# Optimization experiments

Hardware: AMD Instinct MI355X
Metric: run time of the kernel (lower is better)

Reference implementation:

```python
import jax, jax.numpy as jnp
import numpy as np

D_MODEL, NHEAD, INT_DIM = 1024, 16, 4096
HEAD_DIM = D_MODEL // NHEAD
EPS = 1e-5


def _layernorm(x, gamma, beta):
    mu = jnp.mean(x, axis=-1, keepdims=True)
    var = jnp.var(x, axis=-1, keepdims=True)
    return (x - mu) * jax.lax.rsqrt(var + EPS) * gamma + beta


def setup_inputs() -> dict:
    key = jax.random.key(0)
    ks = jax.random.split(key, 16)
    B, T = 2, 2048
    s = 0.02
    inp = {
        'x': jax.random.normal(ks[0], (B, T, D_MODEL), dtype=jnp.float32),
        'Wq': jax.random.normal(ks[1], (D_MODEL, D_MODEL), dtype=jnp.float32) * s,
        'bq': jnp.zeros((D_MODEL,), jnp.float32),
        'Wk': jax.random.normal(ks[2], (D_MODEL, D_MODEL), dtype=jnp.float32) * s,
        'bk': jnp.zeros((D_MODEL,), jnp.float32),
        'Wv': jax.random.normal(ks[3], (D_MODEL, D_MODEL), dtype=jnp.float32) * s,
        'bv': jnp.zeros((D_MODEL,), jnp.float32),
        'Wo': jax.random.normal(ks[4], (D_MODEL, D_MODEL), dtype=jnp.float32) * s,
        'bo': jnp.zeros((D_MODEL,), jnp.float32),
        'ln1_g': jnp.ones((D_MODEL,), jnp.float32),
        'ln1_b': jnp.zeros((D_MODEL,), jnp.float32),
        'ln2_g': jnp.ones((D_MODEL,), jnp.float32),
        'ln2_b': jnp.zeros((D_MODEL,), jnp.float32),
        'W1': jax.random.normal(ks[5], (D_MODEL, INT_DIM), dtype=jnp.float32) * s,
        'b1': jnp.zeros((INT_DIM,), jnp.float32),
        'W2': jax.random.normal(ks[6], (INT_DIM, D_MODEL), dtype=jnp.float32) * s,
        'b2': jnp.zeros((D_MODEL,), jnp.float32),
    }
    return inp


def reference(x, Wq, bq, Wk, bk, Wv, bv, Wo, bo, ln1_g, ln1_b, ln2_g, ln2_b, W1, b1, W2, b2):
    B, T, D = x.shape
    # projections
    q = (x @ Wq + bq).reshape(B, T, NHEAD, HEAD_DIM).transpose(0, 2, 1, 3)
    k = (x @ Wk + bk).reshape(B, T, NHEAD, HEAD_DIM).transpose(0, 2, 1, 3)
    v = (x @ Wv + bv).reshape(B, T, NHEAD, HEAD_DIM).transpose(0, 2, 1, 3)
    # attention: [B,H,T,T] scores, softmax over keys
    scores = jnp.einsum('bhqd,bhkd->bhqk', q, k) / jnp.sqrt(jnp.float32(HEAD_DIM))
    attn = jax.nn.softmax(scores, axis=-1)
    out = jnp.einsum('bhqk,bhkd->bhqd', attn, v)
    out = out.transpose(0, 2, 1, 3).reshape(B, T, D)
    attn_output = out @ Wo + bo
    # residual + layernorm 1
    h = _layernorm(x + attn_output, ln1_g, ln1_b)
    # FFN
    ff = jax.nn.relu(h @ W1 + b1) @ W2 + b2
    # residual + layernorm 2
    return _layernorm(h + ff, ln2_g, ln2_b)
```

## Files before the change

### kernel.cpp

```cpp
#include <hip/hip_runtime.h>
#include <cstdint>

#define DEVI __device__ __forceinline__

typedef float f32x4 __attribute__((ext_vector_type(4)));
typedef __bf16 bf16x8 __attribute__((ext_vector_type(8)));
typedef unsigned int u32x4v __attribute__((ext_vector_type(4)));
typedef unsigned short u16;
typedef unsigned int u32;
typedef unsigned long long u64;

#define LOG2E 1.44269504088896f
#define QSCALE (0.125f * LOG2E)

DEVI u16 bf16bits(float f) {
    u32 u = __builtin_bit_cast(u32, f);
    u32 r = u + 0x7fffu + ((u >> 16) & 1u);
    return (u16)(r >> 16);
}

DEVI float bf2f(u16 v) {
    u32 u = (u32)v << 16;
    return __builtin_bit_cast(float, u);
}

DEVI u32 pack2bf(float a, float b) {
    u16 x = __builtin_bit_cast(u16, (__bf16)a);
    u16 y = __builtin_bit_cast(u16, (__bf16)b);
    return (u32)x | ((u32)y << 16);
}

DEVI float ex2(float x) {
    float r;
    asm("v_exp_f32 %0, %1" : "=v"(r) : "v"(x));
    return r;
}

DEVI void gload16(const void* g, const void* l) {
    __builtin_amdgcn_global_load_lds(
        (const __attribute__((address_space(1))) void*)(u64)(uintptr_t)g,
        (__attribute__((address_space(3))) void*)(u32)(uintptr_t)l,
        16, 0, 0);
}

__global__ __launch_bounds__(256)
void prep_kernel(const float* __restrict__ x, u16* __restrict__ xb,
                 const float* __restrict__ Wq, const float* __restrict__ Wk,
                 const float* __restrict__ Wv, const float* __restrict__ Wo,
                 u16* __restrict__ Wqt, u16* __restrict__ Wkt,
                 u16* __restrict__ Wvt, u16* __restrict__ Wot,
                 const float* __restrict__ W1, u16* __restrict__ W1t,
                 const float* __restrict__ W2, u16* __restrict__ W2t) {
    __shared__ float t[64][65];
    const int b = blockIdx.x;
    const int tid = threadIdx.x;
    if (b < 4096) {
        int i = b * 256 + tid;
        float4 v = ((const float4*)x)[i];
        ((uint2*)xb)[i] = make_uint2(pack2bf(v.x, v.y), pack2bf(v.z, v.w));
        return;
    }
    const float* src;
    u16* dst;
    int K_, N_, k0, n0;
    if (b < 5120) {
        int l = b - 4096;
        int z = l >> 8;
        l &= 255;
        src = z == 0 ? Wq : z == 1 ? Wk : z == 2 ? Wv : Wo;
        dst = z == 0 ? Wqt : z == 1 ? Wkt : z == 2 ? Wvt : Wot;
        K_ = 1024; N_ = 1024;
        k0 = (l & 15) * 64; n0 = (l >> 4) * 64;
    } else if (b < 6144) {
        int l = b - 5120;
        src = W1; dst = W1t; K_ = 1024; N_ = 4096;
        k0 = (l & 15) * 64; n0 = (l >> 4) * 64;
    } else {
        int l = b - 6144;
        src = W2; dst = W2t; K_ = 4096; N_ = 1024;
        k0 = (l & 63) * 64; n0 = (l >> 6) * 64;
    }
#pragma unroll
    for (int i = 0; i < 16; i++) {
        int idx = i * 256 + tid;
        int r = idx >> 6, c = idx & 63;
        t[r][c] = src[(u64)(k0 + r) * N_ + n0 + c];
    }
    __syncthreads();
#pragma unroll
    for (int i = 0; i < 16; i++) {
        int idx = i * 256 + tid;
        int r = idx >> 6, c = idx & 63;
        dst[(u64)(n0 + r) * K_ + k0 + c] = bf16bits(t[c][r]);
    }
}

enum { MODE_QK = 0, MODE_VT = 1, MODE_RESID = 2, MODE_RELU = 3 };

DEVI void gemm_core(const u16* __restrict__ A, const u16* __restrict__ Bt, int K_,
                    u16 (*ldsA)[128 * 64], u16 (*ldsB)[128 * 64],
                    f32x4 (&acc)[4][4], int m0, int n0) {
    const int tid = threadIdx.x;
    const int lane = tid & 63;
    const int wid = tid >> 6;
    const int wr = wid >> 1, wc = wid & 1;
    const int l15 = lane & 15, l4 = lane >> 4;
    const int srow = tid >> 3;
    const int sc = (tid & 7) ^ (srow & 7);

    const u16* ap[4];
    const u16* bp[4];
#pragma unroll
    for (int i = 0; i < 4; i++) {
        ap[i] = A + (u64)(m0 + i * 32 + srow) * K_ + sc * 8;
        bp[i] = Bt + (u64)(n0 + i * 32 + srow) * K_ + sc * 8;
    }

    auto stageA = [&](int buf) {
#pragma unroll
        for (int i = 0; i < 4; i++) {
            gload16(ap[i], (const char*)ldsA[buf] + (i * 256 + tid) * 16);
            ap[i] += 64;
        }
    };
    auto stageB = [&](int buf) {
#pragma unroll
        for (int i = 0; i < 4; i++) {
            gload16(bp[i], (const char*)ldsB[buf] + (i * 256 + tid) * 16);
            bp[i] += 64;
        }
    };

    auto compute = [&](const u16* A_, const u16* B_) {
#pragma unroll
        for (int ks = 0; ks < 2; ks++) {
            bf16x8 af[4], bfr[4];
#pragma unroll
            for (int mi = 0; mi < 4; mi++) {
                int row = wr * 64 + mi * 16 + l15;
                af[mi] = *(const bf16x8*)((const char*)A_ + row * 128 +
                                          (((ks * 4 + l4) ^ (row & 7)) * 16));
            }
#pragma unroll
            for (int ni = 0; ni < 4; ni++) {
                int row = wc * 64 + ni * 16 + l15;
                bfr[ni] = *(const bf16x8*)((const char*)B_ + row * 128 +
                                           (((ks * 4 + l4) ^ (row & 7)) * 16));
            }
            __builtin_amdgcn_s_setprio(1);
#pragma unroll
            for (int mi = 0; mi < 4; mi++)
#pragma unroll
                for (int ni = 0; ni < 4; ni++)
                    acc[mi][ni] = __builtin_amdgcn_mfma_f32_16x16x32_bf16(
                        af[mi], bfr[ni], acc[mi][ni], 0, 0, 0);
            __builtin_amdgcn_s_setprio(0);
        }
    };

    const int nk = K_ >> 6;
    stageA(0);
    stageB(0);
    stageA(1);
    int ca = 0, cbb = 0, sa = 2, sb = 1;
    for (int t = 0; t < nk; t++) {
        if (t < nk - 1) {
            asm volatile("s_waitcnt vmcnt(4)" ::: "memory");
        } else {
            asm volatile("s_waitcnt vmcnt(0)" ::: "memory");
        }
        __builtin_amdgcn_s_barrier();
        if (t + 1 < nk) { stageB(sb); sb ^= 1; }
        if (t + 2 < nk) { stageA(sa); sa = (sa == 2) ? 0 : sa + 1; }
        compute(ldsA[ca], ldsB[cbb]);
        ca = (ca == 2) ? 0 : ca + 1;
        cbb ^= 1;
    }
}

template <int MODE>
DEVI void gemm_epilogue(f32x4 (&acc)[4][4], const float* __restrict__ bias,
                        const float* __restrict__ resid, void* __restrict__ outp,
                        int N_, int m0, int n0, float scale) {
    const int tid = threadIdx.x;
    const int lane = tid & 63;
    const int wid = tid >> 6;
    const int wr = wid >> 1, wc = wid & 1;
    const int l15 = lane & 15, l4 = lane >> 4;
#pragma unroll
    for (int mi = 0; mi < 4; mi++) {
#pragma unroll
        for (int ni = 0; ni < 4; ni++) {
            const int n = n0 + wc * 64 + ni * 16 + l15;
            const float bv = bias[n];
            const int mb = m0 + wr * 64 + mi * 16 + l4 * 4;
            if (MODE == MODE_VT) {
                const int b = mb >> 11, t = mb & 2047;
                const int hh = n >> 6, d = n & 63;
                u32 lo = pack2bf(acc[mi][ni][0] + bv, acc[mi][ni][1] + bv);
                u32 hi = pack2bf(acc[mi][ni][2] + bv, acc[mi][ni][3] + bv);
                u64 idx = ((u64)((b << 4) + hh) * 64 + d) * 2048 + t;
                *(uint2*)((u16*)outp + idx) = make_uint2(lo, hi);
            } else {
#pragma unroll
                for (int r = 0; r < 4; r++) {
                    const int m = mb + r;
                    const float v = acc[mi][ni][r] + bv;
                    if (MODE == MODE_QK) {
                        const int b = m >> 11, t = m & 2047;
                        const int hh = n >> 6, d = n & 63;
                        ((u16*)outp)[(((u64)((b << 4) + hh) * 2048 + t) << 6) + d] =
                            bf16bits(v * scale);
                    } else if (MODE == MODE_RESID) {
                        const u64 i2 = (u64)m * N_ + n;
                        ((float*)outp)[i2] = v + resid[i2];
                    } else {
                        ((u16*)outp)[(u64)m * N_ + n] = bf16bits(fmaxf(v, 0.f));
                    }
                }
            }
        }
    }
}

template <int MODE>
__global__ __launch_bounds__(256, 2)
void gemm_kernel(const u16* __restrict__ A, const u16* __restrict__ Bt,
                 const float* __restrict__ bias, const float* __restrict__ resid,
                 void* __restrict__ outp, int N_, int K_) {
    __shared__ u16 ldsA[3][128 * 64];
    __shared__ u16 ldsB[2][128 * 64];
    const int m0 = blockIdx.x * 128;
    const int n0 = blockIdx.y * 128;
    f32x4 acc[4][4];
#pragma unroll
    for (int i = 0; i < 4; i++)
#pragma unroll
        for (int j = 0; j < 4; j++) acc[i][j] = (f32x4){0.f, 0.f, 0.f, 0.f};
    gemm_core(A, Bt, K_, ldsA, ldsB, acc, m0, n0);
    gemm_epilogue<MODE>(acc, bias, resid, outp, N_, m0, n0, 1.f);
}

__global__ __launch_bounds__(256, 2)
void gemm_qkv_kernel(const u16* __restrict__ A,
                     const u16* __restrict__ Wq, const u16* __restrict__ Wk,
                     const u16* __restrict__ Wv,
                     const float* __restrict__ bq, const float* __restrict__ bk,
                     const float* __restrict__ bv,
                     u16* __restrict__ Qo, u16* __restrict__ Ko, u16* __restrict__ Vo) {
    __shared__ u16 ldsA[3][128 * 64];
    __shared__ u16 ldsB[2][128 * 64];
    const int z = blockIdx.z;
    const u16* Bt = z == 0 ? Wq : z == 1 ? Wk : Wv;
    const float* bias = z == 0 ? bq : z == 1 ? bk : bv;
    const int m0 = blockIdx.x * 128;
    const int n0 = blockIdx.y * 128;
    f32x4 acc[4][4];
#pragma unroll
    for (int i = 0; i < 4; i++)
#pragma unroll
        for (int j = 0; j < 4; j++) acc[i][j] = (f32x4){0.f, 0.f, 0.f, 0.f};
    gemm_core(A, Bt, 1024, ldsA, ldsB, acc, m0, n0);
    if (z == 2)
        gemm_epilogue<MODE_VT>(acc, bias, nullptr, Vo, 1024, m0, n0, 1.f);
    else
        gemm_epilogue<MODE_QK>(acc, bias, nullptr, z == 0 ? Qo : Ko, 1024, m0, n0,
                               z == 0 ? QSCALE : 1.f);
}

template <bool RB16>
__global__ __launch_bounds__(256, 2)
void gemm64_kernel(const u16* __restrict__ A, const u16* __restrict__ Bt,
                   const float* __restrict__ bias, const void* __restrict__ resid,
                   float* __restrict__ outp, int K_) {
    __shared__ u16 ldsA[3][128 * 64];
    __shared__ u16 ldsB[3][64 * 64];
    const int tid = threadIdx.x;
    const int lane = tid & 63;
    const int wid = tid >> 6;
    const int m0 = blockIdx.x * 128;
    const int n0 = blockIdx.y * 64;
    const int l15 = lane & 15, l4 = lane >> 4;
    const int srow = tid >> 3;
    const int sc = (tid & 7) ^ (srow & 7);

    const u16* ap[4];
    const u16* bp[2];
#pragma unroll
    for (int i = 0; i < 4; i++)
        ap[i] = A + (u64)(m0 + i * 32 + srow) * K_ + sc * 8;
#pragma unroll
    for (int i = 0; i < 2; i++)
        bp[i] = Bt + (u64)(n0 + i * 32 + srow) * K_ + sc * 8;

    auto stage = [&](int buf) {
#pragma unroll
        for (int i = 0; i < 4; i++) {
            gload16(ap[i], (const char*)ldsA[buf] + (i * 256 + tid) * 16);
            ap[i] += 64;
        }
#pragma unroll
        for (int i = 0; i < 2; i++) {
            gload16(bp[i], (const char*)ldsB[buf] + (i * 256 + tid) * 16);
            bp[i] += 64;
        }
    };

    f32x4 acc[2][4];
#pragma unroll
    for (int i = 0; i < 2; i++)
#pragma unroll
        for (int j = 0; j < 4; j++) acc[i][j] = (f32x4){0.f, 0.f, 0.f, 0.f};

    auto compute = [&](const u16* A_, const u16* B_) {
#pragma unroll
        for (int ks = 0; ks < 2; ks++) {
            bf16x8 af[2], bfr[4];
#pragma unroll
            for (int mi = 0; mi < 2; mi++) {
                int row = wid * 32 + mi * 16 + l15;
                af[mi] = *(const bf16x8*)((const char*)A_ + row * 128 +
                                          (((ks * 4 + l4) ^ (row & 7)) * 16));
            }
#pragma unroll
            for (int ni = 0; ni < 4; ni++) {
                int row = ni * 16 + l15;
                bfr[ni] = *(const bf16x8*)((const char*)B_ + row * 128 +
                                           (((ks * 4 + l4) ^ (row & 7)) * 16));
            }
            __builtin_amdgcn_s_setprio(1);
#pragma unroll
            for (int mi = 0; mi < 2; mi++)
#pragma unroll
                for (int ni = 0; ni < 4; ni++)
                    acc[mi][ni] = __builtin_amdgcn_mfma_f32_16x16x32_bf16(
                        af[mi], bfr[ni], acc[mi][ni], 0, 0, 0);
            __builtin_amdgcn_s_setprio(0);
        }
    };

    const int nk = K_ >> 6;
    stage(0);
    stage(1);
    int cb = 0, sb = 2;
    for (int t = 0; t < nk; t++) {
        if (t < nk - 1) {
            asm volatile("s_waitcnt vmcnt(6)" ::: "memory");
        } else {
            asm volatile("s_waitcnt vmcnt(0)" ::: "memory");
        }
        __builtin_amdgcn_s_barrier();
        if (t + 2 < nk) stage(sb);
        compute(ldsA[cb], ldsB[cb]);
        cb = (cb == 2) ? 0 : cb + 1;
        sb = (sb == 2) ? 0 : sb + 1;
    }

#pragma unroll
    for (int mi = 0; mi < 2; mi++) {
#pragma unroll
        for (int ni = 0; ni < 4; ni++) {
            const int n = n0 + ni * 16 + l15;
            const float bv = bias[n];
            const int mb = m0 + wid * 32 + mi * 16 + l4 * 4;
#pragma unroll
            for (int r = 0; r < 4; r++) {
                const u64 i2 = (u64)(mb + r) * 1024 + n;
                const float rv = RB16 ? bf2f(((const u16*)resid)[i2])
                                      : ((const float*)resid)[i2];
                outp[i2] = acc[mi][ni][r] + bv + rv;
            }
        }
    }
}

__global__ __launch_bounds__(256, 3)
void attn_kernel(const u16* __restrict__ Qg, const u16* __restrict__ Kg,
                 const u16* __restrict__ Vtg, u16* __restrict__ Og) {
    __shared__ u16 ldsK[3][64 * 64];
    __shared__ u16 ldsV[3][64 * 64];
    const int tid = threadIdx.x;
    const int lane = tid & 63;
    const int w = tid >> 6;
    const int l15 = lane & 15, l4 = lane >> 4;
    const int id = blockIdx.x;
    const int swz = (id & 7) * 128 + (id >> 3);
    const int bh = swz >> 5;
    const int qblk = swz & 31;
    const u64 kvbase = (u64)bh * 2048 * 64;
    const int qw0 = qblk * 64 + w * 16;

    const int srow = tid >> 3;
    const int sc8 = ((tid & 7) ^ (srow & 7)) * 8;
    const u16* kq0 = Kg + kvbase + (u64)srow * 64 + sc8;
    const u16* kq1 = Kg + kvbase + (u64)(srow + 32) * 64 + sc8;
    const u16* vq0 = Vtg + kvbase + (u64)srow * 2048 + sc8;
    const u16* vq1 = Vtg + kvbase + (u64)(srow + 32) * 2048 + sc8;

    auto stage = [&](int buf) {
        gload16(kq0, (const char*)ldsK[buf] + tid * 16);
        gload16(kq1, (const char*)ldsK[buf] + (256 + tid) * 16);
        gload16(vq0, (const char*)ldsV[buf] + tid * 16);
        gload16(vq1, (const char*)ldsV[buf] + (256 + tid) * 16);
        kq0 += 4096; kq1 += 4096; vq0 += 64; vq1 += 64;
    };

    bf16x8 aq[2];
#pragma unroll
    for (int ks = 0; ks < 2; ks++)
        aq[ks] = *(const bf16x8*)(Qg + kvbase + (u64)(qw0 + l15) * 64 + ks * 32 + l4 * 8);
    asm volatile("s_waitcnt vmcnt(0)" ::: "memory");

    stage(0);
    stage(1);

    const u32x4v onesw = {0x3F803F80u, 0x3F803F80u, 0x3F803F80u, 0x3F803F80u};
    const bf16x8 aones = __builtin_bit_cast(bf16x8, onesw);

    f32x4 acco[4];
#pragma unroll
    for (int i = 0; i < 4; i++) acco[i] = (f32x4){0.f, 0.f, 0.f, 0.f};
    f32x4 lacc = (f32x4){0.f, 0.f, 0.f, 0.f};

    auto tile_body = [&](const u16* K_, const u16* V_) {
        f32x4 sf[4];
#pragma unroll
        for (int f = 0; f < 4; f++) sf[f] = (f32x4){0.f, 0.f, 0.f, 0.f};
#pragma unroll
        for (int ks = 0; ks < 2; ks++) {
            bf16x8 ak[4];
#pragma unroll
            for (int f = 0; f < 4; f++) {
                int row = f * 16 + l15;
                ak[f] = *(const bf16x8*)((const char*)K_ + row * 128 +
                                         (((ks * 4 + l4) ^ (row & 7)) * 16));
            }
            __builtin_amdgcn_s_setprio(1);
#pragma unroll
            for (int f = 0; f < 4; f++)
                sf[f] = __builtin_amdgcn_mfma_f32_16x16x32_bf16(ak[f], aq[ks], sf[f], 0, 0, 0);
            __builtin_amdgcn_s_setprio(0);
        }

        u32 A[4], B[4];
#pragma unroll
        for (int f = 0; f < 4; f++) {
            float p0 = ex2(sf[f][0]);
            float p1 = ex2(sf[f][1]);
            float p2 = ex2(sf[f][2]);
            float p3 = ex2(sf[f][3]);
            A[f] = pack2bf(p0, p1);
            B[f] = pack2bf(p2, p3);
        }
        asm volatile("v_permlane32_swap_b32 %0, %1" : "+v"(A[0]), "+v"(A[1]));
        asm volatile("v_permlane16_swap_b32 %0, %1" : "+v"(A[0]), "+v"(A[1]));
        asm volatile("v_permlane32_swap_b32 %0, %1" : "+v"(B[0]), "+v"(B[1]));
        asm volatile("v_permlane16_swap_b32 %0, %1" : "+v"(B[0]), "+v"(B[1]));
        asm volatile("v_permlane32_swap_b32 %0, %1" : "+v"(A[2]), "+v"(A[3]));
        asm volatile("v_permlane16_swap_b32 %0, %1" : "+v"(A[2]), "+v"(A[3]));
        asm volatile("v_permlane32_swap_b32 %0, %1" : "+v"(B[2]), "+v"(B[3]));
        asm volatile("v_permlane16_swap_b32 %0, %1" : "+v"(B[2]), "+v"(B[3]));

#pragma unroll
        for (int ks = 0; ks < 2; ks++) {
            u32x4v pw = {A[2 * ks], B[2 * ks], A[2 * ks + 1], B[2 * ks + 1]};
            bf16x8 pfrag = __builtin_bit_cast(bf16x8, pw);
            bf16x8 av[4];
#pragma unroll
            for (int nf = 0; nf < 4; nf++) {
                int row = nf * 16 + l15;
                av[nf] = *(const bf16x8*)((const char*)V_ + row * 128 +
                                          (((ks * 4 + l4) ^ (row & 7)) * 16));
            }
            __builtin_amdgcn_s_setprio(1);
            lacc = __builtin_amdgcn_mfma_f32_16x16x32_bf16(aones, pfrag, lacc, 0, 0, 0);
#pragma unroll
            for (int nf = 0; nf < 4; nf++)
                acco[nf] = __builtin_amdgcn_mfma_f32_16x16x32_bf16(av[nf], pfrag, acco[nf], 0, 0, 0);
            __builtin_amdgcn_s_setprio(0);
        }
    };

    int cb = 0;
    int sb = 2;
    for (int t = 0; t < 31; t++) {
        asm volatile("s_waitcnt vmcnt(4)" ::: "memory");
        __builtin_amdgcn_s_barrier();
        if (t < 30) stage(sb);
        tile_body(ldsK[cb], ldsV[cb]);
        cb = (cb == 2) ? 0 : cb + 1;
        sb = (sb == 2) ? 0 : sb + 1;
    }
    asm volatile("s_waitcnt vmcnt(0)" ::: "memory");
    __builtin_amdgcn_s_barrier();
    tile_body(ldsK[cb], ldsV[cb]);

    const float inv = 1.f / lacc[0];

    const int b = bh >> 4, h = bh & 15;
    const int tq = qw0 + l15;
#pragma unroll
    for (int nf = 0; nf < 4; nf++) {
        const int d = nf * 16 + l4 * 4;
        u32 lo = pack2bf(acco[nf][0] * inv, acco[nf][1] * inv);
        u32 hi = pack2bf(acco[nf][2] * inv, acco[nf][3] * inv);
        *(uint2*)(Og + ((u64)(b * 2048 + tq) << 10) + h * 64 + d) = make_uint2(lo, hi);
    }
}

template <bool WF32, bool WB16>
__global__ __launch_bounds__(256, 4)
void ln_kernel(const float* __restrict__ in, const float* __restrict__ gam,
               const float* __restrict__ bet, float* __restrict__ outf,
               u16* __restrict__ outb) {
    __shared__ float red[2][4];
    const int row = blockIdx.x;
    const int tid = threadIdx.x;
    float4 v = ((const float4*)(in + (u64)row * 1024))[tid];
    float s = v.x + v.y + v.z + v.w;
    float sq = v.x * v.x + v.y * v.y + v.z * v.z + v.w * v.w;
#pragma unroll
    for (int sh = 1; sh < 64; sh <<= 1) {
        s += __shfl_xor(s, sh, 64);
        sq += __shfl_xor(sq, sh, 64);
    }
    if ((tid & 63) == 0) { red[0][tid >> 6] = s; red[1][tid >> 6] = sq; }
    __syncthreads();
    s = red[0][0] + red[0][1] + red[0][2] + red[0][3];
    sq = red[1][0] + red[1][1] + red[1][2] + red[1][3];
    float mu = s * (1.f / 1024.f);
    float var = sq * (1.f / 1024.f) - mu * mu;
    float inv = rsqrtf(var + 1e-5f);
    float4 g = ((const float4*)gam)[tid];
    float4 bb = ((const float4*)bet)[tid];
    float4 o;
    o.x = (v.x - mu) * inv * g.x + bb.x;
    o.y = (v.y - mu) * inv * g.y + bb.y;
    o.z = (v.z - mu) * inv * g.z + bb.z;
    o.w = (v.w - mu) * inv * g.w + bb.w;
    if (WF32) ((float4*)(outf + (u64)row * 1024))[tid] = o;
    if (WB16) {
        ((uint2*)(outb + (u64)row * 1024))[tid] = make_uint2(pack2bf(o.x, o.y), pack2bf(o.z, o.w));
    }
}

extern "C" void kernel_launch(void* const* d_in, const int* in_sizes, int n_in,
                              void* d_out, int out_size, void* d_ws, size_t ws_size,
                              hipStream_t stream) {
    (void)in_sizes; (void)n_in; (void)out_size; (void)ws_size;
    const float* x  = (const float*)d_in[0];
    const float* Wq = (const float*)d_in[1];
    const float* bq = (const float*)d_in[2];
    const float* Wk = (const float*)d_in[3];
    const float* bk = (const float*)d_in[4];
    const float* Wv = (const float*)d_in[5];
    const float* bv = (const float*)d_in[6];
    const float* Wo = (const float*)d_in[7];
    const float* bo = (const float*)d_in[8];
    const float* g1 = (const float*)d_in[9];
    const float* be1 = (const float*)d_in[10];
    const float* g2 = (const float*)d_in[11];
    const float* be2 = (const float*)d_in[12];
    const float* W1 = (const float*)d_in[13];
    const float* b1 = (const float*)d_in[14];
    const float* W2 = (const float*)d_in[15];
    const float* b2 = (const float*)d_in[16];

    char* ws = (char*)d_ws;
    const u64 MB = 1024ull * 1024ull;
    u16* xb    = (u16*)(ws + 0);
    u16* Wqt   = (u16*)(ws + 8 * MB);
    u16* Wkt   = (u16*)(ws + 10 * MB);
    u16* Wvt   = (u16*)(ws + 12 * MB);
    u16* Wot   = (u16*)(ws + 14 * MB);
    u16* W1t   = (u16*)(ws + 16 * MB);
    u16* W2t   = (u16*)(ws + 24 * MB);
    u16* Qb    = (u16*)(ws + 32 * MB);
    u16* Kb    = (u16*)(ws + 40 * MB);
    u16* Vtb   = (u16*)(ws + 48 * MB);
    u16* Ob    = (u16*)(ws + 56 * MB);
    float* pre1 = (float*)(ws + 64 * MB);
    u16* hb    = (u16*)(ws + 96 * MB);
    u16* ffb   = (u16*)(ws + 104 * MB);
    float* pre2 = (float*)(ws + 80 * MB);

    prep_kernel<<<7168, 256, 0, stream>>>(x, xb, Wq, Wk, Wv, Wo,
                                          Wqt, Wkt, Wvt, Wot, W1, W1t, W2, W2t);

    gemm_qkv_kernel<<<dim3(32, 8, 3), 256, 0, stream>>>(xb, Wqt, Wkt, Wvt,
                                                        bq, bk, bv, Qb, Kb, Vtb);

    attn_kernel<<<1024, 256, 0, stream>>>(Qb, Kb, Vtb, Ob);

    gemm64_kernel<false><<<dim3(32, 16), 256, 0, stream>>>(Ob, Wot, bo, x, pre1, 1024);
    ln_kernel<false, true><<<4096, 256, 0, stream>>>(pre1, g1, be1, nullptr, hb);
    gemm_kernel<MODE_RELU><<<dim3(32, 32), 256, 0, stream>>>(hb, W1t, b1, nullptr, ffb, 4096, 1024);
    gemm64_kernel<true><<<dim3(32, 16), 256, 0, stream>>>(ffb, W2t, b2, hb, pre2, 4096);
    ln_kernel<true, false><<<4096, 256, 0, stream>>>(pre2, g2, be2, (float*)d_out, nullptr);
}
```

Baseline: 202.2 us.

## Stage GEMM epilogues through LDS for coalesced vectorized global stores

GEMM epilogues now write the accumulators into shared memory, reusing the operand LDS buffers, and then read them back in row-contiguous chunks so each thread issues 16-byte global stores. This covers the Q/K/Vt head layouts, the ReLU output and the fp32 residual outputs, and the residual and bias loads become vectorized too. The weight-transpose prep kernel also packs four bf16 values per store instead of writing scalars. The cost is extra barriers and an LDS round trip per tile, with padded strides added to limit bank conflicts.

```diff
diff --git a/kernel.cpp b/kernel.cpp
--- a/kernel.cpp
+++ b/kernel.cpp
@@ -88,14 +88,17 @@
     }
     __syncthreads();
 #pragma unroll
-    for (int i = 0; i < 16; i++) {
+    for (int i = 0; i < 4; i++) {
         int idx = i * 256 + tid;
-        int r = idx >> 6, c = idx & 63;
-        dst[(u64)(n0 + r) * K_ + k0 + c] = bf16bits(t[c][r]);
-    }
-}
-
-enum { MODE_QK = 0, MODE_VT = 1, MODE_RESID = 2, MODE_RELU = 3 };
+        int cq = idx & 15;
+        int r = idx >> 4;
+        u32 lo = (u32)bf16bits(t[cq * 4 + 0][r]) | ((u32)bf16bits(t[cq * 4 + 1][r]) << 16);
+        u32 hi = (u32)bf16bits(t[cq * 4 + 2][r]) | ((u32)bf16bits(t[cq * 4 + 3][r]) << 16);
+        *(uint2*)(dst + (u64)(n0 + r) * K_ + k0 + cq * 4) = make_uint2(lo, hi);
+    }
+}
+
+enum { MODE_QK = 0, MODE_VT = 1, MODE_RELU = 3 };
 
 DEVI void gemm_core(const u16* __restrict__ A, const u16* __restrict__ Bt, int K_,
                     u16 (*ldsA)[128 * 64], u16 (*ldsB)[128 * 64],
@@ -180,45 +183,55 @@
 
 template <int MODE>
 DEVI void gemm_epilogue(f32x4 (&acc)[4][4], const float* __restrict__ bias,
-                        const float* __restrict__ resid, void* __restrict__ outp,
-                        int N_, int m0, int n0, float scale) {
+                        void* __restrict__ outp, int N_, int m0, int n0,
+                        float scale, u16* l16) {
     const int tid = threadIdx.x;
     const int lane = tid & 63;
     const int wid = tid >> 6;
     const int wr = wid >> 1, wc = wid & 1;
     const int l15 = lane & 15, l4 = lane >> 4;
+    __syncthreads();
 #pragma unroll
     for (int mi = 0; mi < 4; mi++) {
 #pragma unroll
         for (int ni = 0; ni < 4; ni++) {
-            const int n = n0 + wc * 64 + ni * 16 + l15;
-            const float bv = bias[n];
-            const int mb = m0 + wr * 64 + mi * 16 + l4 * 4;
+            const int nl = wc * 64 + ni * 16 + l15;
+            const int mlb = wr * 64 + mi * 16 + l4 * 4;
+            const float bv = bias[n0 + nl];
             if (MODE == MODE_VT) {
-                const int b = mb >> 11, t = mb & 2047;
-                const int hh = n >> 6, d = n & 63;
                 u32 lo = pack2bf(acc[mi][ni][0] + bv, acc[mi][ni][1] + bv);
                 u32 hi = pack2bf(acc[mi][ni][2] + bv, acc[mi][ni][3] + bv);
-                u64 idx = ((u64)((b << 4) + hh) * 64 + d) * 2048 + t;
-                *(uint2*)((u16*)outp + idx) = make_uint2(lo, hi);
+                *(uint2*)(l16 + nl * 136 + mlb) = make_uint2(lo, hi);
             } else {
 #pragma unroll
                 for (int r = 0; r < 4; r++) {
-                    const int m = mb + r;
-                    const float v = acc[mi][ni][r] + bv;
-                    if (MODE == MODE_QK) {
-                        const int b = m >> 11, t = m & 2047;
-                        const int hh = n >> 6, d = n & 63;
-                        ((u16*)outp)[(((u64)((b << 4) + hh) * 2048 + t) << 6) + d] =
-                            bf16bits(v * scale);
-                    } else if (MODE == MODE_RESID) {
-                        const u64 i2 = (u64)m * N_ + n;
-                        ((float*)outp)[i2] = v + resid[i2];
-                    } else {
-                        ((u16*)outp)[(u64)m * N_ + n] = bf16bits(fmaxf(v, 0.f));
-                    }
+                    float v = acc[mi][ni][r] + bv;
+                    if (MODE == MODE_RELU) v = fmaxf(v, 0.f);
+                    else v = v * scale;
+                    l16[(mlb + r) * 136 + nl] = bf16bits(v);
                 }
             }
+        }
+    }
+    __syncthreads();
+#pragma unroll
+    for (int it = 0; it < 8; it++) {
+        int c = it * 256 + tid;
+        int rr = c >> 4, nc = c & 15;
+        u32x4v v = *(const u32x4v*)(l16 + rr * 136 + nc * 8);
+        if (MODE == MODE_QK) {
+            int m = m0 + rr;
+            int b = m >> 11, t = m & 2047;
+            int hh = (n0 >> 6) + (nc >> 3);
+            int d = (nc & 7) * 8;
+            *(u32x4v*)((u16*)outp + (((u64)((b << 4) + hh) * 2048 + t) << 6) + d) = v;
+        } else if (MODE == MODE_VT) {
+            int hh = (n0 + rr) >> 6;
+            int d = (n0 + rr) & 63;
+            int b = m0 >> 11, tb = m0 & 2047;
+            *(u32x4v*)((u16*)outp + ((u64)((b << 4) + hh) * 64 + d) * 2048 + tb + nc * 8) = v;
+        } else {
+            *(u32x4v*)((u16*)outp + (u64)(m0 + rr) * N_ + n0 + nc * 8) = v;
         }
     }
 }
@@ -226,8 +239,8 @@
 template <int MODE>
 __global__ __launch_bounds__(256, 2)
 void gemm_kernel(const u16* __restrict__ A, const u16* __restrict__ Bt,
-                 const float* __restrict__ bias, const float* __restrict__ resid,
-                 void* __restrict__ outp, int N_, int K_) {
+                 const float* __restrict__ bias, void* __restrict__ outp,
+                 int N_, int K_) {
     __shared__ u16 ldsA[3][128 * 64];
     __shared__ u16 ldsB[2][128 * 64];
     const int m0 = blockIdx.x * 128;
@@ -238,7 +251,7 @@
 #pragma unroll
         for (int j = 0; j < 4; j++) acc[i][j] = (f32x4){0.f, 0.f, 0.f, 0.f};
     gemm_core(A, Bt, K_, ldsA, ldsB, acc, m0, n0);
-    gemm_epilogue<MODE>(acc, bias, resid, outp, N_, m0, n0, 1.f);
+    gemm_epilogue<MODE>(acc, bias, outp, N_, m0, n0, 1.f, (u16*)ldsA);
 }
 
 __global__ __launch_bounds__(256, 2)
@@ -262,10 +275,10 @@
         for (int j = 0; j < 4; j++) acc[i][j] = (f32x4){0.f, 0.f, 0.f, 0.f};
     gemm_core(A, Bt, 1024, ldsA, ldsB, acc, m0, n0);
     if (z == 2)
-        gemm_epilogue<MODE_VT>(acc, bias, nullptr, Vo, 1024, m0, n0, 1.f);
+        gemm_epilogue<MODE_VT>(acc, bias, Vo, 1024, m0, n0, 1.f, (u16*)ldsA);
     else
-        gemm_epilogue<MODE_QK>(acc, bias, nullptr, z == 0 ? Qo : Ko, 1024, m0, n0,
-                               z == 0 ? QSCALE : 1.f);
+        gemm_epilogue<MODE_QK>(acc, bias, z == 0 ? Qo : Ko, 1024, m0, n0,
+                               z == 0 ? QSCALE : 1.f, (u16*)ldsA);
 }
 
 template <bool RB16>
@@ -356,21 +369,42 @@
         sb = (sb == 2) ? 0 : sb + 1;
     }
 
+    float* fl = (float*)ldsA;
+    __syncthreads();
 #pragma unroll
     for (int mi = 0; mi < 2; mi++) {
 #pragma unroll
         for (int ni = 0; ni < 4; ni++) {
-            const int n = n0 + ni * 16 + l15;
-            const float bv = bias[n];
-            const int mb = m0 + wid * 32 + mi * 16 + l4 * 4;
-#pragma unroll
-            for (int r = 0; r < 4; r++) {
-                const u64 i2 = (u64)(mb + r) * 1024 + n;
-                const float rv = RB16 ? bf2f(((const u16*)resid)[i2])
-                                      : ((const float*)resid)[i2];
-                outp[i2] = acc[mi][ni][r] + bv + rv;
-            }
-        }
+            const int nl = ni * 16 + l15;
+            const int mlb = wid * 32 + mi * 16 + l4 * 4;
+#pragma unroll
+            for (int r = 0; r < 4; r++)
+                fl[(mlb + r) * 68 + nl] = acc[mi][ni][r];
+        }
+    }
+    __syncthreads();
+#pragma unroll
+    for (int it = 0; it < 8; it++) {
+        int c = it * 256 + tid;
+        int rr = c >> 4, nc = c & 15;
+        f32x4 v = *(const f32x4*)(fl + rr * 68 + nc * 4);
+        const int n = n0 + nc * 4;
+        float4 bv = *(const float4*)(bias + n);
+        const u64 i2 = (u64)(m0 + rr) * 1024 + n;
+        float4 rv;
+        if (RB16) {
+            uint2 rb = *(const uint2*)((const u16*)resid + i2);
+            rv.x = bf2f((u16)(rb.x & 0xffffu)); rv.y = bf2f((u16)(rb.x >> 16));
+            rv.z = bf2f((u16)(rb.y & 0xffffu)); rv.w = bf2f((u16)(rb.y >> 16));
+        } else {
+            rv = *(const float4*)((const float*)resid + i2);
+        }
+        float4 o;
+        o.x = v[0] + bv.x + rv.x;
+        o.y = v[1] + bv.y + rv.y;
+        o.z = v[2] + bv.z + rv.z;
+        o.w = v[3] + bv.w + rv.w;
+        *(float4*)(outp + i2) = o;
     }
 }
 
@@ -594,7 +628,7 @@
 
     gemm64_kernel<false><<<dim3(32, 16), 256, 0, stream>>>(Ob, Wot, bo, x, pre1, 1024);
     ln_kernel<false, true><<<4096, 256, 0, stream>>>(pre1, g1, be1, nullptr, hb);
-    gemm_kernel<MODE_RELU><<<dim3(32, 32), 256, 0, stream>>>(hb, W1t, b1, nullptr, ffb, 4096, 1024);
+    gemm_kernel<MODE_RELU><<<dim3(32, 32), 256, 0, stream>>>(hb, W1t, b1, ffb, 4096, 1024);
     gemm64_kernel<true><<<dim3(32, 16), 256, 0, stream>>>(ffb, W2t, b2, hb, pre2, 4096);
     ln_kernel<true, false><<<4096, 256, 0, stream>>>(pre2, g2, be2, (float*)d_out, nullptr);
 }
```

Measured after the change: 202.4 us. No clear change (+0.1%).
